# Kernel tuning notes

Measured on AMD Instinct MI355X. Metric: run time of the kernel, lower is better.

Reference implementation:

```python
import jax, jax.numpy as jnp
import numpy as np
import math

N_HEADS = 16
D_HEAD = 64
D_MODEL = 1024
ROPE_THETA = 10000.0


def setup_inputs() -> dict:
    key = jax.random.key(0)
    k1, k2, k3 = jax.random.split(key, 3)
    B, T = 2, 2048
    x = jax.random.normal(k1, (B, T, D_MODEL), dtype=jnp.float32)
    # torch Linear(in, out) weight has shape (out, in); store transposed (in, out)
    # so forward is x @ w. Scale like default init to keep activations sane.
    w_qkv = jax.random.normal(k2, (D_MODEL, 3 * D_MODEL), dtype=jnp.float32) / math.sqrt(D_MODEL)
    w_o = jax.random.normal(k3, (D_MODEL, D_MODEL), dtype=jnp.float32) / math.sqrt(D_MODEL)
    return {"x": x, "w_qkv": w_qkv, "w_o": w_o}


def _build_rope(T, dtype):
    inv_freq = 1.0 / (ROPE_THETA ** (jnp.arange(0, D_HEAD, 2, dtype=jnp.float32) / D_HEAD))
    t = jnp.arange(T, dtype=jnp.float32)
    freqs = jnp.outer(t, inv_freq)            # [T, D_HEAD/2]
    emb = jnp.concatenate([freqs, freqs], -1)  # [T, D_HEAD]
    return jnp.cos(emb).astype(dtype), jnp.sin(emb).astype(dtype)


def _apply_rope(x, cos, sin):
    # x: [B, T, H, D_HEAD]; cos/sin broadcast as [1, T, 1, D_HEAD]
    x1, x2 = jnp.split(x, 2, axis=-1)
    rotated = jnp.concatenate([-x2, x1], axis=-1)
    return x * cos + rotated * sin


def reference(x, w_qkv, w_o):
    B, T, D = x.shape
    qkv = (x @ w_qkv).reshape(B, T, 3, N_HEADS, D_HEAD)
    q, k, v = qkv[:, :, 0], qkv[:, :, 1], qkv[:, :, 2]  # [B, T, H, Dh]
    cos, sin = _build_rope(T, x.dtype)
    cos = cos[None, :, None, :]
    sin = sin[None, :, None, :]
    q = _apply_rope(q, cos, sin)
    k = _apply_rope(k, cos, sin)
    scale = 1.0 / math.sqrt(D_HEAD)
    # full [B, H, T, T] scores (faithful to the manual matmul-softmax-matmul)
    attn = jnp.einsum("bthd,bshd->bhts", q, k) * scale
    attn = jax.nn.softmax(attn, axis=-1)
    out = jnp.einsum("bhts,bshd->bthd", attn, v).reshape(B, T, D)
    return out @ w_o
```

## Files before the change

kernel.cpp:

```cpp
#include <hip/hip_runtime.h>
#include <cstdint>

typedef unsigned short ushort_t;
typedef __attribute__((ext_vector_type(8))) short v8s;
typedef __attribute__((ext_vector_type(4))) short v4s;
typedef __attribute__((ext_vector_type(2))) unsigned v2u;
typedef __attribute__((ext_vector_type(4))) float v4f;

#define MFMA(a, b, c) __builtin_amdgcn_mfma_f32_16x16x32_bf16(a, b, c, 0, 0, 0)
#define QSCALE 0.18033688011112042f

#define GLL(gp, lp) __builtin_amdgcn_global_load_lds(                        \
    (const __attribute__((address_space(1))) void*)(gp),                     \
    (__attribute__((address_space(3))) void*)(lp), 16, 0, 0)

__device__ __forceinline__ float bf2f(ushort_t u) {
    union { unsigned u; float f; } x; x.u = ((unsigned)u) << 16; return x.f;
}
__device__ __forceinline__ short f2bf(float f) {
    union { float f; unsigned u; } x; x.f = f;
    unsigned r = x.u + 0x7fffu + ((x.u >> 16) & 1u);
    return (short)(r >> 16);
}

__global__ void detect_dtype(const unsigned* __restrict__ x, int* __restrict__ flag) {
    __shared__ int cnt;
    if (threadIdx.x == 0) cnt = 0;
    __syncthreads();
    unsigned w = x[threadIdx.x];
    int e = (w >> 7) & 0xFF;
    int hit = ((e >= 96 && e <= 135) || (w & 0xFFFFu) == 0) ? 1 : 0;
    atomicAdd(&cnt, hit);
    __syncthreads();
    if (threadIdx.x == 0) *flag = (cnt >= 160) ? 1 : 0;
}

__global__ __launch_bounds__(256) void cvt_x(const void* __restrict__ xin,
                                             ushort_t* __restrict__ xb,
                                             const int* __restrict__ flagp, int n8) {
    int i = blockIdx.x * 256 + threadIdx.x;
    if (i >= n8) return;
    if (*flagp) {
        ((v8s*)xb)[i] = ((const v8s*)xin)[i];
    } else {
        const float* xf = (const float*)xin + (size_t)i * 8;
        v8s o;
        #pragma unroll
        for (int j = 0; j < 8; ++j) o[j] = f2bf(xf[j]);
        ((v8s*)xb)[i] = o;
    }
}

__global__ __launch_bounds__(256) void cvt_transpose(const void* __restrict__ in,
                                                     ushort_t* __restrict__ out,
                                                     const int* __restrict__ flagp,
                                                     int R, int C) {
    __shared__ ushort_t tile[32][33];
    int bx = blockIdx.x * 32, by = blockIdx.y * 32;
    int tx = threadIdx.x, ty = threadIdx.y;
    int isbf = *flagp;
    for (int i = ty; i < 32; i += 8) {
        size_t idx = (size_t)(by + i) * C + bx + tx;
        tile[i][tx] = isbf ? ((const ushort_t*)in)[idx]
                           : (ushort_t)f2bf(((const float*)in)[idx]);
    }
    __syncthreads();
    for (int i = ty; i < 32; i += 8) out[(size_t)(bx + i) * R + by + tx] = tile[tx][i];
}

__global__ __launch_bounds__(256) void rope_table(float* __restrict__ tab) {
    int idx = blockIdx.x * 256 + threadIdx.x;
    int t = idx >> 5, d = idx & 31;
    float inv_freq = __expf(-(float)d * 0.28782313662425575f);
    float ang = (float)t * inv_freq;
    float sn, cs;
    sincosf(ang, &sn, &cs);
    tab[t * 64 + d]      = bf2f((ushort_t)f2bf(cs));
    tab[t * 64 + 32 + d] = bf2f((ushort_t)f2bf(sn));
}

template <int MODE>
__global__ __launch_bounds__(256) void gemm_bt(const ushort_t* __restrict__ A,
                                               const ushort_t* __restrict__ BT,
                                               void* __restrict__ C,
                                               const int* __restrict__ flagp,
                                               int M, int N, int K,
                                               ushort_t* __restrict__ Qp,
                                               ushort_t* __restrict__ Kp,
                                               ushort_t* __restrict__ Vp,
                                               const float* __restrict__ tab) {
    __shared__ __align__(16) ushort_t As[128 * 32];
    __shared__ __align__(16) ushort_t Bs[128 * 32];
    int tid = threadIdx.x;
    int lane = tid & 63;
    int lr = lane & 15, lc = lane >> 4;
    int w = tid >> 6;
    int wr = (w >> 1) * 64, wc = (w & 1) * 64;

    int nx = gridDim.x;
    int orig = blockIdx.y * nx + blockIdx.x;
    int cpx = (nx * gridDim.y) >> 3;
    int swz = (orig & 7) * cpx + (orig >> 3);
    int m0 = (swz / nx) * 128, n0 = (swz % nx) * 128;

    int c0 = tid, c1 = tid + 256;
    int r0 = c0 >> 2, s0 = c0 & 3;
    int r1 = c1 >> 2, s1 = c1 & 3;

    const ushort_t* Ag0 = A + (size_t)(m0 + r0) * K + s0 * 8;
    const ushort_t* Ag1 = A + (size_t)(m0 + r1) * K + s1 * 8;
    const ushort_t* Bg0 = BT + (size_t)(n0 + r0) * K + s0 * 8;
    const ushort_t* Bg1 = BT + (size_t)(n0 + r1) * K + s1 * 8;
    ushort_t* Al0 = As + (size_t)(w * 64) * 8;
    ushort_t* Al1 = As + (size_t)(256 + w * 64) * 8;
    ushort_t* Bl0 = Bs + (size_t)(w * 64) * 8;
    ushort_t* Bl1 = Bs + (size_t)(256 + w * 64) * 8;

    v4f acc[4][4] = {};

    for (int kt = 0; kt < K; kt += 32) {
        __syncthreads();
        GLL(Ag0 + kt, Al0);
        GLL(Ag1 + kt, Al1);
        GLL(Bg0 + kt, Bl0);
        GLL(Bg1 + kt, Bl1);
        __syncthreads();

        v8s af[4], bfr[4];
        #pragma unroll
        for (int i = 0; i < 4; ++i)
            af[i] = *(const v8s*)(As + (wr + i * 16 + lr) * 32 + lc * 8);
        #pragma unroll
        for (int j = 0; j < 4; ++j)
            bfr[j] = *(const v8s*)(Bs + (wc + j * 16 + lr) * 32 + lc * 8);
        #pragma unroll
        for (int i = 0; i < 4; ++i)
            #pragma unroll
            for (int j = 0; j < 4; ++j)
                acc[i][j] = MFMA(af[i], bfr[j], acc[i][j]);
    }

    if (MODE == 1) {
        int store_f32 = (*flagp == 0);
        #pragma unroll
        for (int i = 0; i < 4; ++i)
            #pragma unroll
            for (int j = 0; j < 4; ++j)
                #pragma unroll
                for (int r = 0; r < 4; ++r) {
                    int row = m0 + wr + i * 16 + lc * 4 + r;
                    int col = n0 + wc + j * 16 + lr;
                    if (store_f32)
                        ((float*)C)[(size_t)row * N + col] = acc[i][j][r];
                    else
                        ((ushort_t*)C)[(size_t)row * N + col] = (ushort_t)f2bf(acc[i][j][r]);
                }
    } else {
        int region = n0 >> 10;
        int h = ((n0 & 1023) + wc) >> 6;
        if (region < 2) {
            const float sc = (region == 0) ? QSCALE : 1.0f;
            ushort_t* dst = (region == 0) ? Qp : Kp;
            #pragma unroll
            for (int i = 0; i < 4; ++i)
                #pragma unroll
                for (int j = 0; j < 2; ++j) {
                    int d = j * 16 + lr;
                    #pragma unroll
                    for (int r = 0; r < 4; ++r) {
                        int tg = m0 + wr + i * 16 + lc * 4 + r;
                        int b = tg >> 11, tt = tg & 2047;
                        float cs = tab[tt * 64 + d], sn = tab[tt * 64 + 32 + d];
                        float x1 = acc[i][j][r], x2 = acc[i][j + 2][r];
                        size_t base = ((size_t)(b * 16 + h) * 2048 + tt) * 64 + d;
                        dst[base]      = (ushort_t)f2bf((x1 * cs - x2 * sn) * sc);
                        dst[base + 32] = (ushort_t)f2bf((x2 * cs + x1 * sn) * sc);
                    }
                }
        } else {
            #pragma unroll
            for (int i = 0; i < 4; ++i)
                #pragma unroll
                for (int j = 0; j < 4; ++j) {
                    int d = j * 16 + lr;
                    int tg0 = m0 + wr + i * 16 + lc * 4;
                    int b = tg0 >> 11, tt = tg0 & 2047;
                    v4s pk;
                    #pragma unroll
                    for (int r = 0; r < 4; ++r) pk[r] = f2bf(acc[i][j][r]);
                    size_t base = (size_t)(b * 16 + h) * 131072 + (size_t)(tt >> 5) * 2048
                                + (size_t)d * 32 + (tt & 31);
                    *(v4s*)(Vp + base) = pk;
                }
        }
    }
}

__global__ __launch_bounds__(256) void attn(const ushort_t* __restrict__ Qr,
                                            const ushort_t* __restrict__ Kr,
                                            const ushort_t* __restrict__ Vt,
                                            ushort_t* __restrict__ AO) {
    __shared__ __align__(16) char lds[53248];
    int tid = threadIdx.x, lane = tid & 63, W = tid >> 6;
    int lr = lane & 15, lc = lane >> 4;
    int qsub = W & 1, sh = W >> 1;
    int L = blockIdx.x;
    int bh = (L & 7) * 4 + ((L >> 3) & 3);
    int qt = L >> 5;
    int q0 = qt * 128 + qsub * 64;
    int b = bh >> 4, h = bh & 15;
    const ushort_t* Qb = Qr + ((size_t)bh * 2048 + q0) * 64;
    const ushort_t* Kb = Kr + (size_t)bh * 131072 + (size_t)sh * 65536;
    const ushort_t* Vb = Vt + (size_t)bh * 131072 + (size_t)sh * 65536;
    ushort_t* Pw  = (ushort_t*)(lds + 32768 + W * 5120);
    ushort_t* KsG = (ushort_t*)(lds + sh * 16384);
    ushort_t* VsG = (ushort_t*)(lds + sh * 16384 + 8192);

    int gt = tid & 127;
    int c0 = gt, c1 = gt + 128;
    int kr0 = c0 >> 3, kc0 = c0 & 7, kr1 = c1 >> 3, kc1 = c1 & 7;
    const ushort_t* Kg0 = Kb + (size_t)kr0 * 64 + kc0 * 8;
    const ushort_t* Kg1 = Kb + (size_t)kr1 * 64 + kc1 * 8;
    int kl0 = kr0 * 64 + (kc0 ^ (kr0 & 7)) * 8;
    int kl1 = kr1 * 64 + (kc1 ^ (kr1 & 7)) * 8;
    const ushort_t* Vg0 = Vb + (size_t)c0 * 8;
    const ushort_t* Vg1 = Vb + (size_t)c1 * 8;
    int vl0 = c0 * 8, vl1 = c1 * 8;

    v8s qf[4][2];
    #pragma unroll
    for (int jq = 0; jq < 4; ++jq)
        #pragma unroll
        for (int kk = 0; kk < 2; ++kk)
            qf[jq][kk] = *(const v8s*)(Qb + (size_t)(jq * 16 + lr) * 64 + kk * 32 + lc * 8);

    v4f o[4][4] = {};
    float li[4] = {0.f, 0.f, 0.f, 0.f};

    v8s ka = *(const v8s*)(Kg0), kb2 = *(const v8s*)(Kg1);
    v8s va = *(const v8s*)(Vg0), vb2 = *(const v8s*)(Vg1);
    *(v8s*)(KsG + kl0) = ka;
    *(v8s*)(KsG + kl1) = kb2;
    *(v8s*)(VsG + vl0) = va;
    *(v8s*)(VsG + vl1) = vb2;
    ka  = *(const v8s*)(Kg0 + 2048);
    kb2 = *(const v8s*)(Kg1 + 2048);
    va  = *(const v8s*)(Vg0 + 2048);
    vb2 = *(const v8s*)(Vg1 + 2048);
    __syncthreads();

    #pragma unroll 1
    for (int t = 0; t < 32; ++t) {
        int p = t & 1;
        const ushort_t* Kl = KsG + p * 2048;
        const ushort_t* Vl = VsG + p * 2048;

        v8s kf[2][2], vf[4];
        #pragma unroll
        for (int hh = 0; hh < 2; ++hh)
            #pragma unroll
            for (int kk = 0; kk < 2; ++kk)
                kf[hh][kk] = *(const v8s*)(Kl + (hh * 16 + lr) * 64 + (((kk * 4 + lc) ^ (lr & 7)) * 8));
        #pragma unroll
        for (int i = 0; i < 4; ++i)
            vf[i] = *(const v8s*)(Vl + (i * 16 + lr) * 32 + lc * 8);

        v4f St[2][4] = {};
        __builtin_amdgcn_s_setprio(1);
        #pragma unroll
        for (int hh = 0; hh < 2; ++hh)
            #pragma unroll
            for (int jq = 0; jq < 4; ++jq) {
                St[hh][jq] = MFMA(kf[hh][0], qf[jq][0], St[hh][jq]);
                St[hh][jq] = MFMA(kf[hh][1], qf[jq][1], St[hh][jq]);
            }
        __builtin_amdgcn_s_setprio(0);

        if (t + 1 < 32) {
            ushort_t* Kn = KsG + (p ^ 1) * 2048;
            ushort_t* Vn = VsG + (p ^ 1) * 2048;
            *(v8s*)(Kn + kl0) = ka;
            *(v8s*)(Kn + kl1) = kb2;
            *(v8s*)(Vn + vl0) = va;
            *(v8s*)(Vn + vl1) = vb2;
        }
        if (t + 2 < 32) {
            ka  = *(const v8s*)(Kg0 + (size_t)(t + 2) * 2048);
            kb2 = *(const v8s*)(Kg1 + (size_t)(t + 2) * 2048);
            va  = *(const v8s*)(Vg0 + (size_t)(t + 2) * 2048);
            vb2 = *(const v8s*)(Vg1 + (size_t)(t + 2) * 2048);
        }

        #pragma unroll
        for (int jq = 0; jq < 4; ++jq)
            #pragma unroll
            for (int hh = 0; hh < 2; ++hh) {
                #pragma unroll
                for (int r = 0; r < 4; ++r) {
                    float ev = __builtin_amdgcn_exp2f(St[hh][jq][r]);
                    St[hh][jq][r] = ev;
                    li[jq] += ev;
                }
                unsigned d0 = __builtin_amdgcn_perm(__float_as_uint(St[hh][jq][1]),
                                                    __float_as_uint(St[hh][jq][0]), 0x07060302u);
                unsigned d1 = __builtin_amdgcn_perm(__float_as_uint(St[hh][jq][3]),
                                                    __float_as_uint(St[hh][jq][2]), 0x07060302u);
                v2u pk = {d0, d1};
                *(v2u*)(Pw + (jq * 16 + lr) * 40 + hh * 16 + lc * 4) = pk;
            }
        __builtin_amdgcn_s_waitcnt(0xc07f);
        __builtin_amdgcn_s_setprio(1);
        #pragma unroll
        for (int jq = 0; jq < 4; ++jq) {
            v8s pf = *(const v8s*)(Pw + (jq * 16 + lr) * 40 + lc * 8);
            #pragma unroll
            for (int i = 0; i < 4; ++i)
                o[i][jq] = MFMA(vf[i], pf, o[i][jq]);
        }
        __builtin_amdgcn_s_setprio(0);
        __syncthreads();
    }

    #pragma unroll
    for (int jq = 0; jq < 4; ++jq) {
        li[jq] += __shfl_xor(li[jq], 16);
        li[jq] += __shfl_xor(li[jq], 32);
    }
    float* MO = (float*)(lds + qsub * 17408);
    float* Ml = (float*)(lds + 34816 + qsub * 256);
    __syncthreads();
    if (sh == 1) {
        #pragma unroll
        for (int jq = 0; jq < 4; ++jq) {
            #pragma unroll
            for (int i = 0; i < 4; ++i)
                *(v4f*)(MO + (jq * 16 + lr) * 68 + i * 16 + lc * 4) = o[i][jq];
            if (lc == 0) Ml[jq * 16 + lr] = li[jq];
        }
    }
    __syncthreads();
    if (sh == 0) {
        #pragma unroll
        for (int jq = 0; jq < 4; ++jq) {
            float inv = 1.0f / (li[jq] + Ml[jq * 16 + lr]);
            int t = q0 + jq * 16 + lr;
            #pragma unroll
            for (int i = 0; i < 4; ++i) {
                v4f m = *(const v4f*)(MO + (jq * 16 + lr) * 68 + i * 16 + lc * 4);
                v4s pk;
                #pragma unroll
                for (int r = 0; r < 4; ++r) pk[r] = f2bf((o[i][jq][r] + m[r]) * inv);
                *(v4s*)(AO + (size_t)(b * 2048 + t) * 1024 + h * 64 + i * 16 + lc * 4) = pk;
            }
        }
    }
}

extern "C" void kernel_launch(void* const* d_in, const int* in_sizes, int n_in,
                              void* d_out, int out_size, void* d_ws, size_t ws_size,
                              hipStream_t stream) {
    char* ws = (char*)d_ws;
    int*      flag  = (int*)ws;
    ushort_t* wqkvT = (ushort_t*)(ws + 256);
    ushort_t* woT   = (ushort_t*)(ws + 6291712);
    ushort_t* xb    = (ushort_t*)(ws + 8388864);
    ushort_t* Qr    = (ushort_t*)(ws + 16777472);
    ushort_t* Kr    = (ushort_t*)(ws + 25166080);
    ushort_t* Vt    = (ushort_t*)(ws + 33554688);
    ushort_t* AO    = (ushort_t*)(ws + 41943296);
    float*    tab   = (float*)(ws + 50331904);

    detect_dtype<<<1, 256, 0, stream>>>((const unsigned*)d_in[0], flag);
    rope_table<<<256, 256, 0, stream>>>(tab);
    cvt_x<<<2048, 256, 0, stream>>>(d_in[0], xb, flag, 524288);
    dim3 tb(32, 8);
    cvt_transpose<<<dim3(96, 32), tb, 0, stream>>>(d_in[1], wqkvT, flag, 1024, 3072);
    cvt_transpose<<<dim3(32, 32), tb, 0, stream>>>(d_in[2], woT, flag, 1024, 1024);
    gemm_bt<2><<<dim3(24, 32), 256, 0, stream>>>(xb, wqkvT, nullptr, flag, 4096, 3072, 1024,
                                                 Qr, Kr, Vt, tab);
    attn<<<512, 256, 0, stream>>>(Qr, Kr, Vt, AO);
    gemm_bt<1><<<dim3(8, 32), 256, 0, stream>>>(AO, woT, d_out, flag, 4096, 1024, 1024,
                                                nullptr, nullptr, nullptr, nullptr);
}
```

Before: 209.3 us.

## Double-buffer GEMM LDS loads, narrow output-projection tiles, merge small prep kernels

The GEMM now uses double-buffered shared memory. It prefetches the next K tile with global_load_lds while the current tile feeds MFMA, so one barrier per iteration is removed and load latency can overlap compute. The output-projection GEMM gets a BN=64 template variant with twice as many blocks, to improve CU occupancy on a grid that was previously 256 blocks. The dtype detection and rope table kernels are merged into one launch, and the two weight transposes into another, to cut launch overhead. Shared memory use doubles, which may lower occupancy.

```diff
diff --git a/kernel.cpp b/kernel.cpp
--- a/kernel.cpp
+++ b/kernel.cpp
@@ -23,16 +23,28 @@
     return (short)(r >> 16);
 }
 
-__global__ void detect_dtype(const unsigned* __restrict__ x, int* __restrict__ flag) {
-    __shared__ int cnt;
-    if (threadIdx.x == 0) cnt = 0;
-    __syncthreads();
-    unsigned w = x[threadIdx.x];
-    int e = (w >> 7) & 0xFF;
-    int hit = ((e >= 96 && e <= 135) || (w & 0xFFFFu) == 0) ? 1 : 0;
-    atomicAdd(&cnt, hit);
-    __syncthreads();
-    if (threadIdx.x == 0) *flag = (cnt >= 160) ? 1 : 0;
+__global__ void detect_rope(const unsigned* __restrict__ x, int* __restrict__ flag,
+                            float* __restrict__ tab) {
+    if (blockIdx.x == 0) {
+        __shared__ int cnt;
+        if (threadIdx.x == 0) cnt = 0;
+        __syncthreads();
+        unsigned w = x[threadIdx.x];
+        int e = (w >> 7) & 0xFF;
+        int hit = ((e >= 96 && e <= 135) || (w & 0xFFFFu) == 0) ? 1 : 0;
+        atomicAdd(&cnt, hit);
+        __syncthreads();
+        if (threadIdx.x == 0) *flag = (cnt >= 160) ? 1 : 0;
+    } else {
+        int idx = (blockIdx.x - 1) * 256 + threadIdx.x;
+        int t = idx >> 5, d = idx & 31;
+        float inv_freq = __expf(-(float)d * 0.28782313662425575f);
+        float ang = (float)t * inv_freq;
+        float sn, cs;
+        sincosf(ang, &sn, &cs);
+        tab[t * 64 + d]      = bf2f((ushort_t)f2bf(cs));
+        tab[t * 64 + 32 + d] = bf2f((ushort_t)f2bf(sn));
+    }
 }
 
 __global__ __launch_bounds__(256) void cvt_x(const void* __restrict__ xin,
@@ -51,12 +63,17 @@
     }
 }
 
-__global__ __launch_bounds__(256) void cvt_transpose(const void* __restrict__ in,
-                                                     ushort_t* __restrict__ out,
-                                                     const int* __restrict__ flagp,
-                                                     int R, int C) {
+__global__ __launch_bounds__(256) void cvt_transpose2(const void* __restrict__ in1,
+                                                      const void* __restrict__ in2,
+                                                      ushort_t* __restrict__ out1,
+                                                      ushort_t* __restrict__ out2,
+                                                      const int* __restrict__ flagp) {
     __shared__ ushort_t tile[32][33];
-    int bx = blockIdx.x * 32, by = blockIdx.y * 32;
+    const void* in; ushort_t* out; int C, bx;
+    if (blockIdx.x < 96) { in = in1; out = out1; C = 3072; bx = blockIdx.x * 32; }
+    else                 { in = in2; out = out2; C = 1024; bx = (blockIdx.x - 96) * 32; }
+    const int R = 1024;
+    int by = blockIdx.y * 32;
     int tx = threadIdx.x, ty = threadIdx.y;
     int isbf = *flagp;
     for (int i = ty; i < 32; i += 8) {
@@ -68,18 +85,7 @@
     for (int i = ty; i < 32; i += 8) out[(size_t)(bx + i) * R + by + tx] = tile[tx][i];
 }
 
-__global__ __launch_bounds__(256) void rope_table(float* __restrict__ tab) {
-    int idx = blockIdx.x * 256 + threadIdx.x;
-    int t = idx >> 5, d = idx & 31;
-    float inv_freq = __expf(-(float)d * 0.28782313662425575f);
-    float ang = (float)t * inv_freq;
-    float sn, cs;
-    sincosf(ang, &sn, &cs);
-    tab[t * 64 + d]      = bf2f((ushort_t)f2bf(cs));
-    tab[t * 64 + 32 + d] = bf2f((ushort_t)f2bf(sn));
-}
-
-template <int MODE>
+template <int MODE, int BN>
 __global__ __launch_bounds__(256) void gemm_bt(const ushort_t* __restrict__ A,
                                                const ushort_t* __restrict__ BT,
                                                void* __restrict__ C,
@@ -89,19 +95,20 @@
                                                ushort_t* __restrict__ Kp,
                                                ushort_t* __restrict__ Vp,
                                                const float* __restrict__ tab) {
-    __shared__ __align__(16) ushort_t As[128 * 32];
-    __shared__ __align__(16) ushort_t Bs[128 * 32];
+    constexpr int NJ = BN / 32;
+    __shared__ __align__(16) ushort_t As[2][128 * 32];
+    __shared__ __align__(16) ushort_t Bs[2][BN * 32];
     int tid = threadIdx.x;
     int lane = tid & 63;
     int lr = lane & 15, lc = lane >> 4;
     int w = tid >> 6;
-    int wr = (w >> 1) * 64, wc = (w & 1) * 64;
+    int wr = (w >> 1) * 64, wc = (w & 1) * (BN / 2);
 
     int nx = gridDim.x;
     int orig = blockIdx.y * nx + blockIdx.x;
     int cpx = (nx * gridDim.y) >> 3;
     int swz = (orig & 7) * cpx + (orig >> 3);
-    int m0 = (swz / nx) * 128, n0 = (swz % nx) * 128;
+    int m0 = (swz / nx) * 128, n0 = (swz % nx) * BN;
 
     int c0 = tid, c1 = tid + 256;
     int r0 = c0 >> 2, s0 = c0 & 3;
@@ -111,33 +118,44 @@
     const ushort_t* Ag1 = A + (size_t)(m0 + r1) * K + s1 * 8;
     const ushort_t* Bg0 = BT + (size_t)(n0 + r0) * K + s0 * 8;
     const ushort_t* Bg1 = BT + (size_t)(n0 + r1) * K + s1 * 8;
-    ushort_t* Al0 = As + (size_t)(w * 64) * 8;
-    ushort_t* Al1 = As + (size_t)(256 + w * 64) * 8;
-    ushort_t* Bl0 = Bs + (size_t)(w * 64) * 8;
-    ushort_t* Bl1 = Bs + (size_t)(256 + w * 64) * 8;
-
-    v4f acc[4][4] = {};
-
+    const int aoff0 = w * 512;
+    const int aoff1 = 2048 + w * 512;
+    const int boff0 = w * 512;
+    const int boff1 = 2048 + w * 512;
+
+    v4f acc[4][NJ] = {};
+
+    GLL(Ag0, &As[0][aoff0]);
+    GLL(Ag1, &As[0][aoff1]);
+    GLL(Bg0, &Bs[0][boff0]);
+    if constexpr (BN == 128) GLL(Bg1, &Bs[0][boff1]);
+    __syncthreads();
+
+    int buf = 0;
     for (int kt = 0; kt < K; kt += 32) {
+        if (kt + 32 < K) {
+            int nb = buf ^ 1;
+            GLL(Ag0 + kt + 32, &As[nb][aoff0]);
+            GLL(Ag1 + kt + 32, &As[nb][aoff1]);
+            GLL(Bg0 + kt + 32, &Bs[nb][boff0]);
+            if constexpr (BN == 128) GLL(Bg1 + kt + 32, &Bs[nb][boff1]);
+        }
+
+        v8s af[4], bfr[NJ];
+        #pragma unroll
+        for (int i = 0; i < 4; ++i)
+            af[i] = *(const v8s*)(&As[buf][0] + (wr + i * 16 + lr) * 32 + lc * 8);
+        #pragma unroll
+        for (int j = 0; j < NJ; ++j)
+            bfr[j] = *(const v8s*)(&Bs[buf][0] + (wc + j * 16 + lr) * 32 + lc * 8);
+        #pragma unroll
+        for (int i = 0; i < 4; ++i)
+            #pragma unroll
+            for (int j = 0; j < NJ; ++j)
+                acc[i][j] = MFMA(af[i], bfr[j], acc[i][j]);
+
         __syncthreads();
-        GLL(Ag0 + kt, Al0);
-        GLL(Ag1 + kt, Al1);
-        GLL(Bg0 + kt, Bl0);
-        GLL(Bg1 + kt, Bl1);
-        __syncthreads();
-
-        v8s af[4], bfr[4];
-        #pragma unroll
-        for (int i = 0; i < 4; ++i)
-            af[i] = *(const v8s*)(As + (wr + i * 16 + lr) * 32 + lc * 8);
-        #pragma unroll
-        for (int j = 0; j < 4; ++j)
-            bfr[j] = *(const v8s*)(Bs + (wc + j * 16 + lr) * 32 + lc * 8);
-        #pragma unroll
-        for (int i = 0; i < 4; ++i)
-            #pragma unroll
-            for (int j = 0; j < 4; ++j)
-                acc[i][j] = MFMA(af[i], bfr[j], acc[i][j]);
+        buf ^= 1;
     }
 
     if (MODE == 1) {
@@ -145,7 +163,7 @@
         #pragma unroll
         for (int i = 0; i < 4; ++i)
             #pragma unroll
-            for (int j = 0; j < 4; ++j)
+            for (int j = 0; j < NJ; ++j)
                 #pragma unroll
                 for (int r = 0; r < 4; ++r) {
                     int row = m0 + wr + i * 16 + lc * 4 + r;
@@ -171,7 +189,7 @@
                         int tg = m0 + wr + i * 16 + lc * 4 + r;
                         int b = tg >> 11, tt = tg & 2047;
                         float cs = tab[tt * 64 + d], sn = tab[tt * 64 + 32 + d];
-                        float x1 = acc[i][j][r], x2 = acc[i][j + 2][r];
+                        float x1 = acc[i][j][r], x2 = acc[i][(j + 2) % NJ][r];
                         size_t base = ((size_t)(b * 16 + h) * 2048 + tt) * 64 + d;
                         dst[base]      = (ushort_t)f2bf((x1 * cs - x2 * sn) * sc);
                         dst[base + 32] = (ushort_t)f2bf((x2 * cs + x1 * sn) * sc);
@@ -181,7 +199,7 @@
             #pragma unroll
             for (int i = 0; i < 4; ++i)
                 #pragma unroll
-                for (int j = 0; j < 4; ++j) {
+                for (int j = 0; j < NJ; ++j) {
                     int d = j * 16 + lr;
                     int tg0 = m0 + wr + i * 16 + lc * 4;
                     int b = tg0 >> 11, tt = tg0 & 2047;
@@ -370,15 +388,13 @@
     ushort_t* AO    = (ushort_t*)(ws + 41943296);
     float*    tab   = (float*)(ws + 50331904);
 
-    detect_dtype<<<1, 256, 0, stream>>>((const unsigned*)d_in[0], flag);
-    rope_table<<<256, 256, 0, stream>>>(tab);
+    detect_rope<<<257, 256, 0, stream>>>((const unsigned*)d_in[0], flag, tab);
     cvt_x<<<2048, 256, 0, stream>>>(d_in[0], xb, flag, 524288);
     dim3 tb(32, 8);
-    cvt_transpose<<<dim3(96, 32), tb, 0, stream>>>(d_in[1], wqkvT, flag, 1024, 3072);
-    cvt_transpose<<<dim3(32, 32), tb, 0, stream>>>(d_in[2], woT, flag, 1024, 1024);
-    gemm_bt<2><<<dim3(24, 32), 256, 0, stream>>>(xb, wqkvT, nullptr, flag, 4096, 3072, 1024,
-                                                 Qr, Kr, Vt, tab);
+    cvt_transpose2<<<dim3(128, 32), tb, 0, stream>>>(d_in[1], d_in[2], wqkvT, woT, flag);
+    gemm_bt<2, 128><<<dim3(24, 32), 256, 0, stream>>>(xb, wqkvT, nullptr, flag, 4096, 3072, 1024,
+                                                      Qr, Kr, Vt, tab);
     attn<<<512, 256, 0, stream>>>(Qr, Kr, Vt, AO);
-    gemm_bt<1><<<dim3(8, 32), 256, 0, stream>>>(AO, woT, d_out, flag, 4096, 1024, 1024,
-                                                nullptr, nullptr, nullptr, nullptr);
-}
+    gemm_bt<1, 64><<<dim3(16, 32), 256, 0, stream>>>(AO, woT, d_out, flag, 4096, 1024, 1024,
+                                                     nullptr, nullptr, nullptr, nullptr);
+}
```

Measured after the change: 191.6 us. -8.5%, faster.
